# Kernel optimization log

Measured on AMD Instinct MI355X. Metric: run time of the kernel, lower is better.

Reference implementation:

```python
import jax, jax.numpy as jnp
import numpy as np

B, V, T = 8, 25, 128
C, NH, DK = 256, 8, 32      # hidden_size = NH*DK; dv == dk (required by residual shapes)
DFF, IT = 1024, 4           # FFN hidden (d_in), num_layers
EPS_LN, EPS_BN, SLOPE = 1e-6, 1e-5, 0.01
SCALE = np.float32(1.0 / np.sqrt(DK))


def setup_inputs():
    ks = iter(jax.random.split(jax.random.key(0), 40))
    def w(shape, s=0.05):
        return jax.random.normal(next(ks), shape, jnp.float32) * s
    inp = {'data': jax.random.normal(next(ks), (B, C, V, T), jnp.float32)}
    inp['ln_g'] = jnp.ones((IT, C)); inp['ln_b'] = jnp.zeros((IT, C))
    for p in ('tj', 'tr'):
        for nm in ('q', 'k', 'v'):
            inp[p + '_w' + nm] = w((IT, C, C))
            inp[p + '_b' + nm] = jnp.zeros((IT, C))
        inp[p + '_bn_g'] = jnp.ones((IT, C)); inp[p + '_bn_b'] = jnp.zeros((IT, C))
        inp[p + '_w1'] = w((IT, DFF, C)); inp[p + '_b1'] = jnp.zeros((IT, DFF))
        inp[p + '_w2'] = w((IT, C, DFF)); inp[p + '_b2'] = jnp.zeros((IT, C))
        inp[p + '_fbn_g'] = jnp.ones((IT, C)); inp[p + '_fbn_b'] = jnp.zeros((IT, C))
    return inp


def _bn(x, g, b, axes):
    # train-mode BatchNorm: batch stats, biased variance; channel axis = 1
    m = x.mean(axes, keepdims=True)
    v = ((x - m) ** 2).mean(axes, keepdims=True)
    sh = [1] * x.ndim; sh[1] = -1
    return (x - m) * jax.lax.rsqrt(v + EPS_BN) * g.reshape(sh) + b.reshape(sh)


def _ffn(x, w1, b1, w2, b2, fg, fb):
    # PositionFeedForward on x: [N, C, L] -> [N, C, L]
    xt = jnp.swapaxes(x, 1, 2)                                   # [N, L, C]
    h = jax.nn.relu(jnp.einsum('nlc,fc->nlf', xt, w1) + b1)
    o = jnp.einsum('nlf,cf->nlc', h, w2) + b2 + xt               # residual
    return _bn(jnp.swapaxes(o, 1, 2), fg, fb, (0, 2))


def _tju(x, ax, wq, bq, wk, bk, wv, bv, bn_g, bn_b, w1, b1, w2, b2, fg, fb):
    # sliding-window (3) self-attn + 2 relay tokens; x: [N,C,T], ax: [N,C,2,T]
    N = x.shape[0]
    q = (jnp.einsum('oc,nct->not', wq, x) + bq[:, None]).reshape(N, NH, DK, T)
    k = (jnp.einsum('oc,nct->not', wk, x) + bk[:, None]).reshape(N, NH, DK, T)
    v = (jnp.einsum('oc,nct->not', wv, x) + bv[:, None]).reshape(N, NH, DK, T)
    kp = jnp.pad(k, ((0, 0), (0, 0), (0, 0), (1, 1)))
    vp = jnp.pad(v, ((0, 0), (0, 0), (0, 0), (1, 1)))
    kw = jnp.stack([kp[..., u:u + T] for u in range(3)], axis=3)  # [N,NH,DK,3,T]
    vw = jnp.stack([vp[..., u:u + T] for u in range(3)], axis=3)
    ak = (jnp.einsum('oc,ncat->noat', wk, ax) + bk[:, None, None]).reshape(N, NH, DK, 2, T)
    av = (jnp.einsum('oc,ncat->noat', wv, ax) + bv[:, None, None]).reshape(N, NH, DK, 2, T)
    kk = jnp.concatenate([kw, ak], axis=3)                        # [N,NH,DK,5,T]
    vv = jnp.concatenate([vw, av], axis=3)
    a = jax.nn.softmax(jnp.einsum('nhdt,nhdwt->nhwt', q, kk) * SCALE, axis=2)
    att = jnp.einsum('nhwt,nhdwt->nhdt', a, vv).reshape(N, C, T)
    ret = _bn(x + att, bn_g, bn_b, (0, 2))
    return _ffn(ret, w1, b1, w2, b2, fg, fb)


def _tru(r, y, wq, bq, wk, bk, wv, bv, bn_g, bn_b, w1, b1, w2, b2, fg, fb):
    # relay cross-attention; r: [N,C], y: [N,C,L]
    N, _, L = y.shape
    q = (r @ wq.T + bq).reshape(N, NH, DK)
    k = (jnp.einsum('oc,ncl->nol', wk, y) + bk[:, None]).reshape(N, NH, DK, L)
    v = (jnp.einsum('oc,ncl->nol', wv, y) + bv[:, None]).reshape(N, NH, DK, L)
    a = jax.nn.softmax(jnp.einsum('nhd,nhdl->nhl', q, k) * SCALE, axis=-1)
    att = jnp.einsum('nhl,nhdl->nhd', a, v).reshape(N, C)
    ret = _bn((r + att)[:, :, None], bn_g, bn_b, (0, 2))          # BN over batch
    return _ffn(ret, w1, b1, w2, b2, fg, fb)[:, :, 0]


def _forward(data, ln_g, ln_b, tj, tr):
    N = B * V
    embs = jnp.transpose(data, (0, 2, 1, 3)).reshape(N, C, T)
    nodes, relay = embs, embs.mean(2)                             # relay: [N,C]
    for i in range(IT):
        ax = jnp.concatenate([embs[:, :, None, :],
                              jnp.broadcast_to(relay[:, :, None, None], (N, C, 1, T))], axis=2)
        m = nodes.mean(1, keepdims=True)
        vv = nodes.var(1, keepdims=True)
        xln = (nodes - m) * jax.lax.rsqrt(vv + EPS_LN) * ln_g[i][None, :, None] + ln_b[i][None, :, None]
        nodes = jax.nn.leaky_relu(_tju(xln, ax, *[p[i] for p in tj]), SLOPE)
        y = jnp.concatenate([relay[:, :, None], nodes], axis=2)   # [N,C,T+1]
        relay = jax.nn.leaky_relu(_tru(relay, y, *[p[i] for p in tr]), SLOPE)
    return nodes.reshape(B, V, C, T)


def reference(data, ln_g, ln_b,
              tj_wq, tj_bq, tj_wk, tj_bk, tj_wv, tj_bv, tj_bn_g, tj_bn_b,
              tj_w1, tj_b1, tj_w2, tj_b2, tj_fbn_g, tj_fbn_b,
              tr_wq, tr_bq, tr_wk, tr_bk, tr_wv, tr_bv, tr_bn_g, tr_bn_b,
              tr_w1, tr_b1, tr_w2, tr_b2, tr_fbn_g, tr_fbn_b):
    tj = (tj_wq, tj_bq, tj_wk, tj_bk, tj_wv, tj_bv, tj_bn_g, tj_bn_b,
          tj_w1, tj_b1, tj_w2, tj_b2, tj_fbn_g, tj_fbn_b)
    tr = (tr_wq, tr_bq, tr_wk, tr_bk, tr_wv, tr_bv, tr_bn_g, tr_bn_b,
          tr_w1, tr_b1, tr_w2, tr_b2, tr_fbn_g, tr_fbn_b)
    return _forward(data, ln_g, ln_b, tj, tr)
```

## Files before the change

### kernel.cpp

```cpp
#include <hip/hip_runtime.h>
#include <cstddef>

#define BB   8
#define VV   25
#define TT   128
#define CC   256
#define NHH  8
#define DKK  32
#define DFFF 1024
#define ITER 4
#define NN   (BB*VV)
#define NT   (NN*TT)
#define LL1  (TT+1)
#define EPS_LN 1e-6f
#define EPS_BN 1e-5f
#define SLOPE  0.01f
#define SCALE_F 0.17677669529663687f

typedef unsigned short ushort_t;
typedef __attribute__((ext_vector_type(8))) short short8;
typedef __attribute__((ext_vector_type(4))) short short4_t;
typedef __attribute__((ext_vector_type(4))) float floatx4;

union U8 { short8 v; ushort_t u[8]; };

__device__ __forceinline__ float bf2f(ushort_t u) {
    union { unsigned int i; float f; } x; x.i = ((unsigned int)u) << 16; return x.f;
}
__device__ __forceinline__ ushort_t f2bf(float f) {
    union { float f; unsigned int i; } x; x.f = f;
    unsigned int r = x.i + 0x7FFFu + ((x.i >> 16) & 1u);
    return (ushort_t)(r >> 16);
}
__device__ __forceinline__ float2 bn_fin(float s, float ss) {
    float m = s * (1.0f/NT);
    float var = ss * (1.0f/NT) - m*m; if (var < 0.f) var = 0.f;
    return make_float2(m, rsqrtf(var + EPS_BN));
}

__device__ __forceinline__ void gl_lds16(const ushort_t* g, ushort_t* l) {
    __builtin_amdgcn_global_load_lds(
        (const __attribute__((address_space(1))) unsigned int*)g,
        (__attribute__((address_space(3))) unsigned int*)l,
        16, 0, 0);
}

__device__ __forceinline__ void ld32(const ushort_t* p, float* q) {
    #pragma unroll
    for (int c8 = 0; c8 < 4; c8++) {
        U8 u; u.v = *(const short8*)(p + c8*8);
        #pragma unroll
        for (int j = 0; j < 8; j++) q[c8*8+j] = bf2f(u.u[j]);
    }
}
__device__ __forceinline__ float dot32(const ushort_t* p, const float* q) {
    float s = 0.f;
    #pragma unroll
    for (int c8 = 0; c8 < 4; c8++) {
        U8 u; u.v = *(const short8*)(p + c8*8);
        #pragma unroll
        for (int j = 0; j < 8; j++) s += q[c8*8+j]*bf2f(u.u[j]);
    }
    return s;
}
__device__ __forceinline__ void acc32(const ushort_t* p, float e, float* av) {
    #pragma unroll
    for (int c8 = 0; c8 < 4; c8++) {
        U8 u; u.v = *(const short8*)(p + c8*8);
        #pragma unroll
        for (int j = 0; j < 8; j++) av[c8*8+j] += e*bf2f(u.u[j]);
    }
}

__global__ __launch_bounds__(256) void k_zero(float* __restrict__ p, int n)
{
    int i = blockIdx.x*256 + threadIdx.x;
    if (i < n) p[i] = 0.f;
}
__global__ __launch_bounds__(256) void k_cast2(const float* __restrict__ src,
    ushort_t* __restrict__ dst, int per, int dstride, int total)
{
    int i = blockIdx.x*256 + threadIdx.x;
    if (i < total) dst[(size_t)(i/per)*dstride + (i%per)] = f2bf(src[i]);
}
__global__ __launch_bounds__(256) void k_copy2(const float* __restrict__ src,
    float* __restrict__ dst, int per, int dstride, int total)
{
    int i = blockIdx.x*256 + threadIdx.x;
    if (i < total) dst[(size_t)(i/per)*dstride + (i%per)] = src[i];
}

__global__ __launch_bounds__(128) void k_embed(const float* __restrict__ data,
    float* __restrict__ nodesf, ushort_t* __restrict__ embs_bf, float* __restrict__ relay)
{
    __shared__ float tile[32][TT+1];
    int cc0 = blockIdx.x*32, n = blockIdx.y;
    int b = n / VV, v = n % VV, t = threadIdx.x;
    for (int cl = 0; cl < 32; cl++)
        tile[cl][t] = data[(((size_t)b*CC + cc0 + cl)*VV + v)*TT + t];
    __syncthreads();
    if (t < 32) {
        float s = 0.f;
        for (int tt = 0; tt < TT; tt++) s += tile[t][tt];
        relay[n*CC + cc0 + t] = s * (1.0f/TT);
    }
    #pragma unroll 8
    for (int it = 0; it < 32; it++) {
        int t_l = it*4 + (t >> 5), c_l = t & 31;
        float val = tile[c_l][t_l];
        size_t o = (size_t)(n*TT + t_l)*CC + cc0 + c_l;
        nodesf[o] = val;
        embs_bf[o] = f2bf(val);
    }
}

__global__ __launch_bounds__(256) void k_layernorm(float* __restrict__ x,
    ushort_t* __restrict__ outb, const float* __restrict__ g, const float* __restrict__ b)
{
    int wave = threadIdx.x >> 6, lane = threadIdx.x & 63;
    size_t base = (size_t)(blockIdx.x*4 + wave)*CC + lane*4;
    float4 v = *(float4*)&x[base];
    float s  = v.x + v.y + v.z + v.w;
    float ss = v.x*v.x + v.y*v.y + v.z*v.z + v.w*v.w;
    #pragma unroll
    for (int o = 32; o; o >>= 1) { s += __shfl_xor(s, o); ss += __shfl_xor(ss, o); }
    float m = s * (1.0f/CC);
    float var = ss * (1.0f/CC) - m*m; if (var < 0.f) var = 0.f;
    float rs = rsqrtf(var + EPS_LN);
    float4 gg = *(const float4*)&g[lane*4];
    float4 bb = *(const float4*)&b[lane*4];
    v.x = (v.x - m)*rs*gg.x + bb.x;
    v.y = (v.y - m)*rs*gg.y + bb.y;
    v.z = (v.z - m)*rs*gg.z + bb.z;
    v.w = (v.w - m)*rs*gg.w + bb.w;
    *(float4*)&x[base] = v;
    ushort_t o4[4] = {f2bf(v.x), f2bf(v.y), f2bf(v.z), f2bf(v.w)};
    *(short4_t*)&outb[base] = *(short4_t*)o4;
}

#define FL_RELU  1
#define FL_BF16  2
#define FL_RESBN 4

#define STAGE(SA, SB, T_) do {                                              \
    gl_lds16(aSrc[0] + (T_)*32, &SA[dstOff[0]]);                            \
    gl_lds16(bSrc[0] + (T_)*32, &SB[dstOff[0]]);                            \
    gl_lds16(aSrc[1] + (T_)*32, &SA[dstOff[1]]);                            \
    gl_lds16(bSrc[1] + (T_)*32, &SB[dstOff[1]]);                            \
    } while (0)

#define COMPUTE(SA, SB) do {                                                \
    short8 af_[4], bf_[4];                                                  \
    _Pragma("unroll")                                                       \
    for (int mi_ = 0; mi_ < 4; mi_++)                                       \
        af_[mi_] = *(const short8*)&SA[aOff[mi_]];                          \
    _Pragma("unroll")                                                       \
    for (int ni_ = 0; ni_ < 4; ni_++)                                       \
        bf_[ni_] = *(const short8*)&SB[bOff[ni_]];                          \
    _Pragma("unroll")                                                       \
    for (int mi_ = 0; mi_ < 4; mi_++)                                       \
        _Pragma("unroll")                                                   \
        for (int ni_ = 0; ni_ < 4; ni_++)                                   \
            acc[mi_][ni_] = __builtin_amdgcn_mfma_f32_16x16x32_bf16(        \
                bf_[ni_], af_[mi_], acc[mi_][ni_], 0, 0, 0);                \
    } while (0)

#define PHASE(CA, CB, PA, PB, T_) do {                                      \
    if ((T_) + 2 < NK) STAGE(PA, PB, (T_) + 2);                             \
    COMPUTE(CA, CB);                                                        \
    if ((T_) + 1 < NK) {                                                    \
        __builtin_amdgcn_sched_barrier(0);                                  \
        if ((T_) + 2 < NK)                                                  \
            asm volatile("s_waitcnt vmcnt(4) lgkmcnt(0)" ::: "memory");     \
        else                                                                \
            asm volatile("s_waitcnt vmcnt(0) lgkmcnt(0)" ::: "memory");     \
        __builtin_amdgcn_s_barrier();                                       \
        __builtin_amdgcn_sched_barrier(0);                                  \
    }                                                                       \
    } while (0)

template<int K>
__global__ __launch_bounds__(256) void k_gemm_mfma(
    const ushort_t* __restrict__ A, const ushort_t* __restrict__ B,
    const float* __restrict__ bias,
    const float* rx, const float* __restrict__ rawms,
    const float* __restrict__ bng, const float* __restrict__ bnb,
    float* outf, ushort_t* __restrict__ outb,
    int ostride, int ntiles_n, int flags)
{
    __shared__ ushort_t sA0[128*32];
    __shared__ ushort_t sB0[128*32];
    __shared__ ushort_t sA1[128*32];
    __shared__ ushort_t sB1[128*32];
    __shared__ ushort_t sA2[128*32];
    __shared__ ushort_t sB2[128*32];
    const int pid = blockIdx.x;
    const int xcd = pid & 7, idx = pid >> 3;
    const int n0 = (idx % ntiles_n) * 128;
    const int m0 = (xcd*25 + idx/ntiles_n) * 128;
    const int tid = threadIdx.x;
    const int lane = tid & 63, wave = tid >> 6;
    const int wm = (wave & 1) * 64, wn = (wave >> 1) * 64;
    const int fr = lane >> 4, fc = lane & 15;

    const ushort_t* aSrc[2];
    const ushort_t* bSrc[2];
    int dstOff[2];
    #pragma unroll
    for (int j = 0; j < 2; j++) {
        int s = wave*128 + j*64 + lane;
        int row = s >> 2;
        int kcs = ((s & 3) - (row >> 1)) & 3;
        aSrc[j] = A + (size_t)(m0 + row)*K + kcs*8;
        bSrc[j] = B + (size_t)(n0 + row)*K + kcs*8;
        dstOff[j] = (wave*128 + j*64)*8;
    }
    int aOff[4], bOff[4];
    #pragma unroll
    for (int mi = 0; mi < 4; mi++) {
        int row = wm + mi*16 + fc;
        aOff[mi] = row*32 + (((fr + (row >> 1)) & 3) * 8);
    }
    #pragma unroll
    for (int ni = 0; ni < 4; ni++) {
        int row = wn + ni*16 + fc;
        bOff[ni] = row*32 + (((fr + (row >> 1)) & 3) * 8);
    }

    floatx4 acc[4][4];
    #pragma unroll
    for (int i = 0; i < 4; i++)
        #pragma unroll
        for (int j = 0; j < 4; j++) acc[i][j] = (floatx4){0.f,0.f,0.f,0.f};

    constexpr int NK = K >> 5;
    STAGE(sA0, sB0, 0);
    if (NK > 1) STAGE(sA1, sB1, 1);
    __builtin_amdgcn_sched_barrier(0);
    if (NK > 1) asm volatile("s_waitcnt vmcnt(4)" ::: "memory");
    else        asm volatile("s_waitcnt vmcnt(0)" ::: "memory");
    __builtin_amdgcn_s_barrier();
    __builtin_amdgcn_sched_barrier(0);

    #pragma unroll
    for (int tb = 0; tb < NK; tb += 3) {
        PHASE(sA0, sB0, sA2, sB2, tb);
        if (tb + 1 < NK) PHASE(sA1, sB1, sA0, sB0, tb + 1);
        if (tb + 2 < NK) PHASE(sA2, sB2, sA1, sB1, tb + 2);
    }

    #pragma unroll
    for (int ni = 0; ni < 4; ni++) {
        int nb = n0 + wn + ni*16 + fr*4;
        float4 bias4 = *(const float4*)&bias[nb];
        float bm[4] = {0,0,0,0}, bs[4] = {0,0,0,0}, bb2[4] = {0,0,0,0};
        if (flags & FL_RESBN) {
            float4 s1 = *(const float4*)&rawms[nb];
            float4 s2 = *(const float4*)&rawms[CC + nb];
            float4 g4 = *(const float4*)&bng[nb];
            float4 b4 = *(const float4*)&bnb[nb];
            float2 f0 = bn_fin(s1.x, s2.x); float2 f1 = bn_fin(s1.y, s2.y);
            float2 f2 = bn_fin(s1.z, s2.z); float2 f3 = bn_fin(s1.w, s2.w);
            bm[0]=f0.x; bm[1]=f1.x; bm[2]=f2.x; bm[3]=f3.x;
            bs[0]=f0.y*g4.x; bs[1]=f1.y*g4.y; bs[2]=f2.y*g4.z; bs[3]=f3.y*g4.w;
            bb2[0]=b4.x; bb2[1]=b4.y; bb2[2]=b4.z; bb2[3]=b4.w;
        }
        float bia[4] = {bias4.x, bias4.y, bias4.z, bias4.w};
        #pragma unroll
        for (int mi = 0; mi < 4; mi++) {
            int m = m0 + wm + mi*16 + fc;
            size_t idx2 = (size_t)m*ostride + nb;
            float vals[4];
            #pragma unroll
            for (int r = 0; r < 4; r++) vals[r] = acc[mi][ni][r] + bia[r];
            if (flags & FL_RESBN) {
                float4 rx4 = *(const float4*)&rx[idx2];
                float rxa[4] = {rx4.x, rx4.y, rx4.z, rx4.w};
                #pragma unroll
                for (int r = 0; r < 4; r++)
                    vals[r] += (rxa[r] - bm[r])*bs[r] + bb2[r];
            }
            if (flags & FL_RELU)
                #pragma unroll
                for (int r = 0; r < 4; r++) vals[r] = fmaxf(vals[r], 0.f);
            if (flags & FL_BF16) {
                ushort_t o4[4] = {f2bf(vals[0]), f2bf(vals[1]),
                                  f2bf(vals[2]), f2bf(vals[3])};
                *(short4_t*)&outb[idx2] = *(short4_t*)o4;
            } else {
                float4 ov = make_float4(vals[0], vals[1], vals[2], vals[3]);
                *(float4*)&outf[idx2] = ov;
            }
        }
    }
}

__global__ __launch_bounds__(256) void k_sgemm(
    const float* __restrict__ W, const float* __restrict__ X,
    const float* __restrict__ bias, const float* __restrict__ res,
    float* __restrict__ out, int K, int OUT, int do_relu)
{
    __shared__ float sW[16][260];
    __shared__ float sX[16][260];
    int o0 = blockIdx.x*16, n0 = blockIdx.y*16;
    int tx = threadIdx.x, ty = threadIdx.y;
    int tid = ty*16 + tx;
    float acc0 = 0.f, acc1 = 0.f;
    for (int kc = 0; kc < K; kc += 256) {
        #pragma unroll
        for (int j = 0; j < 4; j++) {
            int lin = tid + j*256;
            int row = lin >> 6, c4 = (lin & 63)*4;
            *(float4*)&sW[row][c4] = *(const float4*)&W[(size_t)(o0+row)*K + kc + c4];
            float4 xv = make_float4(0.f,0.f,0.f,0.f);
            if (n0 + row < NN) xv = *(const float4*)&X[(size_t)(n0+row)*K + kc + c4];
            *(float4*)&sX[row][c4] = xv;
        }
        __syncthreads();
        #pragma unroll 8
        for (int k4 = 0; k4 < 64; k4 += 2) {
            float4 w0 = *(const float4*)&sW[tx][k4*4];
            float4 x0 = *(const float4*)&sX[ty][k4*4];
            float4 w1 = *(const float4*)&sW[tx][k4*4+4];
            float4 x1 = *(const float4*)&sX[ty][k4*4+4];
            acc0 += w0.x*x0.x + w0.y*x0.y + w0.z*x0.z + w0.w*x0.w;
            acc1 += w1.x*x1.x + w1.y*x1.y + w1.z*x1.z + w1.w*x1.w;
        }
        __syncthreads();
    }
    float accv = acc0 + acc1;
    int o = o0 + tx, n = n0 + ty;
    if (n < NN) {
        float val = accv + bias[o];
        if (res) val += res[(size_t)n*OUT + o];
        if (do_relu) val = fmaxf(val, 0.f);
        out[(size_t)n*OUT + o] = val;
    }
}

__global__ __launch_bounds__(128) void k_attn_tj(
    const ushort_t* __restrict__ qkv, const ushort_t* __restrict__ ekv,
    const float* __restrict__ rel, const float* __restrict__ xln,
    float* __restrict__ out)
{
    int t = threadIdx.x, h = blockIdx.x, n = blockIdx.y;
    int nt = n*TT + t;
    const ushort_t* qp = qkv + (size_t)nt*768 + h*32;
    const ushort_t* kp = qp + 256;
    const ushort_t* vp = qp + 512;
    const ushort_t* ep = ekv + (size_t)nt*512 + h*32;
    const float*    rp = rel + n*1280 + h*32;

    float qv[32];
    ld32(qp, qv);
    float s0 = 0.f, s1, s2 = 0.f, s3, s4 = 0.f;
    s1 = dot32(kp, qv);
    s3 = dot32(ep, qv);
    #pragma unroll
    for (int j = 0; j < 8; j++) {
        float4 rv4 = *(const float4*)&rp[j*4];
        s4 += qv[j*4]*rv4.x + qv[j*4+1]*rv4.y + qv[j*4+2]*rv4.z + qv[j*4+3]*rv4.w;
    }
    if (t > 0)    s0 = dot32(kp - 768, qv);
    if (t < TT-1) s2 = dot32(kp + 768, qv);

    s0 *= SCALE_F; s1 *= SCALE_F; s2 *= SCALE_F; s3 *= SCALE_F; s4 *= SCALE_F;
    float mx = fmaxf(fmaxf(fmaxf(s0, s1), fmaxf(s2, s3)), s4);
    float e0 = expf(s0-mx), e1 = expf(s1-mx), e2 = expf(s2-mx), e3 = expf(s3-mx), e4 = expf(s4-mx);
    float inv = 1.f/(e0+e1+e2+e3+e4);
    e0 *= inv; e1 *= inv; e2 *= inv; e3 *= inv; e4 *= inv;

    float av[32];
    #pragma unroll
    for (int d = 0; d < 32; d++) av[d] = 0.f;
    acc32(vp, e1, av);
    acc32(ep + 256, e3, av);
    if (t > 0)    acc32(vp - 768, e0, av);
    if (t < TT-1) acc32(vp + 768, e2, av);
    #pragma unroll
    for (int j = 0; j < 8; j++) {
        float4 rv4 = *(const float4*)&rp[256 + j*4];
        av[j*4] += e4*rv4.x; av[j*4+1] += e4*rv4.y; av[j*4+2] += e4*rv4.z; av[j*4+3] += e4*rv4.w;
    }
    const float* xp = xln + (size_t)nt*CC + h*32;
    float* op = out + (size_t)nt*CC + h*32;
    #pragma unroll
    for (int j = 0; j < 8; j++) {
        float4 xv = *(const float4*)&xp[j*4];
        float4 ov;
        ov.x = xv.x + av[j*4]; ov.y = xv.y + av[j*4+1];
        ov.z = xv.z + av[j*4+2]; ov.w = xv.w + av[j*4+3];
        *(float4*)&op[j*4] = ov;
    }
}

__global__ __launch_bounds__(256) void k_bnstats_tm(const float* __restrict__ x,
    float* __restrict__ accum)
{
    __shared__ float lds[8][256];
    int w = threadIdx.x >> 6, lane = threadIdx.x & 63;
    size_t base = (size_t)blockIdx.x*TT*CC;
    float s[4] = {0,0,0,0}, ss[4] = {0,0,0,0};
    for (int tok = w; tok < TT; tok += 4) {
        float4 v = *(const float4*)&x[base + (size_t)tok*CC + lane*4];
        s[0] += v.x; s[1] += v.y; s[2] += v.z; s[3] += v.w;
        ss[0] += v.x*v.x; ss[1] += v.y*v.y; ss[2] += v.z*v.z; ss[3] += v.w*v.w;
    }
    #pragma unroll
    for (int j = 0; j < 4; j++) { lds[w][lane*4+j] = s[j]; lds[4+w][lane*4+j] = ss[j]; }
    __syncthreads();
    int c = threadIdx.x;
    float ps  = lds[0][c]+lds[1][c]+lds[2][c]+lds[3][c];
    float pss = lds[4][c]+lds[5][c]+lds[6][c]+lds[7][c];
    atomicAdd(&accum[c], ps);
    atomicAdd(&accum[CC + c], pss);
}

__global__ __launch_bounds__(256) void k_bn_apply_raw(const float* __restrict__ x,
    const float* __restrict__ acc, const float* __restrict__ g, const float* __restrict__ b,
    ushort_t* __restrict__ outb)
{
    size_t base = ((size_t)blockIdx.x*256 + threadIdx.x)*4;
    int c0 = (int)(base & (CC-1));
    float4 v  = *(const float4*)&x[base];
    float4 a1 = *(const float4*)&acc[c0];
    float4 a2 = *(const float4*)&acc[CC + c0];
    float4 g4 = *(const float4*)&g[c0];
    float4 b4 = *(const float4*)&b[c0];
    float vals[4] = {v.x,v.y,v.z,v.w};
    float s1v[4] = {a1.x,a1.y,a1.z,a1.w};
    float s2v[4] = {a2.x,a2.y,a2.z,a2.w};
    float gg[4] = {g4.x,g4.y,g4.z,g4.w};
    float bb[4] = {b4.x,b4.y,b4.z,b4.w};
    ushort_t o4[4];
    #pragma unroll
    for (int j = 0; j < 4; j++) {
        float2 f = bn_fin(s1v[j], s2v[j]);
        o4[j] = f2bf((vals[j] - f.x)*f.y*gg[j] + bb[j]);
    }
    *(short4_t*)&outb[base] = *(short4_t*)o4;
}

__global__ __launch_bounds__(256) void k_bn_ln(const float* __restrict__ x,
    const float* __restrict__ acc, const float* __restrict__ fg, const float* __restrict__ fb,
    const float* __restrict__ lg, const float* __restrict__ lb,
    float* __restrict__ xlnf, ushort_t* __restrict__ xlnb, ushort_t* __restrict__ nodesb)
{
    int wave = threadIdx.x >> 6, lane = threadIdx.x & 63;
    int c0 = lane*4;
    size_t base = (size_t)(blockIdx.x*4 + wave)*CC + c0;
    float4 v  = *(const float4*)&x[base];
    float4 a1 = *(const float4*)&acc[c0];
    float4 a2 = *(const float4*)&acc[CC + c0];
    float4 g4 = *(const float4*)&fg[c0];
    float4 b4 = *(const float4*)&fb[c0];
    float vals[4] = {v.x,v.y,v.z,v.w};
    float s1v[4] = {a1.x,a1.y,a1.z,a1.w};
    float s2v[4] = {a2.x,a2.y,a2.z,a2.w};
    float gg[4] = {g4.x,g4.y,g4.z,g4.w};
    float bb[4] = {b4.x,b4.y,b4.z,b4.w};
    ushort_t nb4[4];
    #pragma unroll
    for (int j = 0; j < 4; j++) {
        float2 f = bn_fin(s1v[j], s2v[j]);
        float vv = (vals[j] - f.x)*f.y*gg[j] + bb[j];
        vv = vv > 0.f ? vv : SLOPE*vv;
        vals[j] = vv;
        nb4[j] = f2bf(vv);
    }
    *(short4_t*)&nodesb[base] = *(short4_t*)nb4;
    float s  = vals[0]+vals[1]+vals[2]+vals[3];
    float ss = vals[0]*vals[0]+vals[1]*vals[1]+vals[2]*vals[2]+vals[3]*vals[3];
    #pragma unroll
    for (int o = 32; o; o >>= 1) { s += __shfl_xor(s, o); ss += __shfl_xor(ss, o); }
    float m = s * (1.0f/CC);
    float var = ss * (1.0f/CC) - m*m; if (var < 0.f) var = 0.f;
    float rs = rsqrtf(var + EPS_LN);
    float4 lg4 = *(const float4*)&lg[c0];
    float4 lb4 = *(const float4*)&lb[c0];
    float lgv[4] = {lg4.x,lg4.y,lg4.z,lg4.w};
    float lbv[4] = {lb4.x,lb4.y,lb4.z,lb4.w};
    float4 xo;
    ushort_t xb4[4];
    float t0 = (vals[0]-m)*rs*lgv[0] + lbv[0];
    float t1 = (vals[1]-m)*rs*lgv[1] + lbv[1];
    float t2 = (vals[2]-m)*rs*lgv[2] + lbv[2];
    float t3 = (vals[3]-m)*rs*lgv[3] + lbv[3];
    xo.x = t0; xo.y = t1; xo.z = t2; xo.w = t3;
    xb4[0]=f2bf(t0); xb4[1]=f2bf(t1); xb4[2]=f2bf(t2); xb4[3]=f2bf(t3);
    *(float4*)&xlnf[base] = xo;
    *(short4_t*)&xlnb[base] = *(short4_t*)xb4;
}

__global__ __launch_bounds__(256) void k_bn_out_t(const float* __restrict__ x,
    const float* __restrict__ acc, const float* __restrict__ g, const float* __restrict__ b,
    float* __restrict__ out)
{
    __shared__ float tile[64][65];
    int nt0 = blockIdx.x*64, c0 = blockIdx.y*64;
    int w = threadIdx.x >> 6, lane = threadIdx.x & 63;
    int n = nt0 >> 7, t0 = nt0 & 127;
    int c = c0 + lane;
    float2 f = bn_fin(acc[c], acc[CC + c]);
    float gg = f.y*g[c], mm = f.x, bb = b[c];
    #pragma unroll
    for (int it = 0; it < 16; it++) {
        int tok = it*4 + w;
        float v = x[(size_t)(nt0 + tok)*CC + c];
        v = (v - mm)*gg + bb;
        v = v > 0.f ? v : SLOPE*v;
        tile[tok][lane] = v;
    }
    __syncthreads();
    #pragma unroll
    for (int it = 0; it < 16; it++) {
        int c_l = it*4 + w;
        out[(size_t)(n*CC + c0 + c_l)*TT + t0 + lane] = tile[lane][c_l];
    }
}

__global__ __launch_bounds__(64) void k_bn_relay(const float* __restrict__ x,
    float* __restrict__ out, const float* __restrict__ g, const float* __restrict__ b, int leaky)
{
    int c = blockIdx.x, tid = threadIdx.x;
    float s = 0.f, ss = 0.f;
    for (int n = tid; n < NN; n += 64) { float v = x[(size_t)n*CC + c]; s += v; ss += v*v; }
    for (int off = 32; off; off >>= 1) { s += __shfl_down(s, off); ss += __shfl_down(ss, off); }
    float S = __shfl(s, 0), SS = __shfl(ss, 0);
    float m = S / NN;
    float var = SS / NN - m*m; if (var < 0.f) var = 0.f;
    float rs = rsqrtf(var + EPS_BN);
    float gg = g[c]*rs, bb = b[c];
    for (int n = tid; n < NN; n += 64) {
        float v = (x[(size_t)n*CC + c] - m)*gg + bb;
        if (leaky) v = v > 0.f ? v : SLOPE*v;
        out[(size_t)n*CC + c] = v;
    }
}

__global__ __launch_bounds__(64) void k_attn_tr(
    const float* __restrict__ rel, const float* __restrict__ ykv,
    const float* __restrict__ relay, float* __restrict__ out)
{
    int h = blockIdx.x, n = blockIdx.y, tid = threadIdx.x;
    __shared__ float sc[LL1];
    __shared__ float red[64][33];
    float q0[32];
    const float* qp = rel + (size_t)n*1280 + 1024 + h*32;
    #pragma unroll
    for (int j = 0; j < 8; j++) {
        float4 v = *(const float4*)&qp[j*4];
        q0[j*4] = v.x; q0[j*4+1] = v.y; q0[j*4+2] = v.z; q0[j*4+3] = v.w;
    }
    for (int l = tid; l < LL1; l += 64) {
        const float* kp = (l == 0) ? (rel + (size_t)n*1280 + 512 + h*32)
                                   : (ykv + (size_t)(n*TT + l-1)*512 + h*32);
        float s = 0.f;
        #pragma unroll
        for (int j = 0; j < 8; j++) {
            float4 v = *(const float4*)&kp[j*4];
            s += q0[j*4]*v.x + q0[j*4+1]*v.y + q0[j*4+2]*v.z + q0[j*4+3]*v.w;
        }
        sc[l] = s * SCALE_F;
    }
    __syncthreads();
    float mx = -1e30f;
    for (int l = tid; l < LL1; l += 64) mx = fmaxf(mx, sc[l]);
    for (int off = 32; off; off >>= 1) mx = fmaxf(mx, __shfl_xor(mx, off));
    float sum = 0.f;
    for (int l = tid; l < LL1; l += 64) { float e = expf(sc[l]-mx); sc[l] = e; sum += e; }
    for (int off = 32; off; off >>= 1) sum += __shfl_xor(sum, off);
    __syncthreads();
    float av[32];
    #pragma unroll
    for (int d = 0; d < 32; d++) av[d] = 0.f;
    for (int l = tid; l < LL1; l += 64) {
        float e = sc[l];
        const float* vp = (l == 0) ? (rel + (size_t)n*1280 + 768 + h*32)
                                   : (ykv + (size_t)(n*TT + l-1)*512 + 256 + h*32);
        #pragma unroll
        for (int j = 0; j < 8; j++) {
            float4 v = *(const float4*)&vp[j*4];
            av[j*4] += e*v.x; av[j*4+1] += e*v.y; av[j*4+2] += e*v.z; av[j*4+3] += e*v.w;
        }
    }
    #pragma unroll
    for (int d = 0; d < 32; d++) red[tid][d] = av[d];
    __syncthreads();
    if (tid < 32) {
        float a = 0.f;
        for (int k = 0; k < 64; k++) a += red[k][tid];
        a /= sum;
        int idx = n*CC + h*32 + tid;
        out[idx] = relay[idx] + a;
    }
}

extern "C" void kernel_launch(void* const* d_in, const int* in_sizes, int n_in,
                              void* d_out, int out_size, void* d_ws, size_t ws_size,
                              hipStream_t stream)
{
    const float* data    = (const float*)d_in[0];
    const float* ln_g    = (const float*)d_in[1];
    const float* ln_b    = (const float*)d_in[2];
    const float* tj_wq   = (const float*)d_in[3];
    const float* tj_bq   = (const float*)d_in[4];
    const float* tj_wk   = (const float*)d_in[5];
    const float* tj_bk   = (const float*)d_in[6];
    const float* tj_wv   = (const float*)d_in[7];
    const float* tj_bv   = (const float*)d_in[8];
    const float* tj_bn_g = (const float*)d_in[9];
    const float* tj_bn_b = (const float*)d_in[10];
    const float* tj_w1   = (const float*)d_in[11];
    const float* tj_b1   = (const float*)d_in[12];
    const float* tj_w2   = (const float*)d_in[13];
    const float* tj_b2   = (const float*)d_in[14];
    const float* tj_fbn_g= (const float*)d_in[15];
    const float* tj_fbn_b= (const float*)d_in[16];
    const float* tr_wq   = (const float*)d_in[17];
    const float* tr_bq   = (const float*)d_in[18];
    const float* tr_wk   = (const float*)d_in[19];
    const float* tr_bk   = (const float*)d_in[20];
    const float* tr_wv   = (const float*)d_in[21];
    const float* tr_bv   = (const float*)d_in[22];
    const float* tr_bn_g = (const float*)d_in[23];
    const float* tr_bn_b = (const float*)d_in[24];
    const float* tr_w1   = (const float*)d_in[25];
    const float* tr_b1   = (const float*)d_in[26];
    const float* tr_w2   = (const float*)d_in[27];
    const float* tr_b2   = (const float*)d_in[28];
    const float* tr_fbn_g= (const float*)d_in[29];
    const float* tr_fbn_b= (const float*)d_in[30];

    const size_t SZ = (size_t)NT*CC;
    const size_t SZ_NC = (size_t)NN*CC;

    float* ws = (float*)d_ws;
    size_t off = 0;
    auto alloc = [&](size_t nf) { float* p = ws + off; off += nf; return p; };
    float*    nodesf  = alloc(SZ);
    float*    sbuf    = alloc(SZ);
    float*    P1      = alloc(SZ*5/2);
    ushort_t* xs_bf   = (ushort_t*)alloc(SZ/2);
    ushort_t* embs_bf = (ushort_t*)alloc(SZ/2);
    ushort_t* nb_bf   = (ushort_t*)alloc(SZ/2);
    float* accs   = alloc(8*512);
    float* relayA = alloc(SZ_NC);
    float* relayB = alloc(SZ_NC);
    float* rel    = alloc((size_t)NN*1280);
    float* ret0   = alloc(SZ_NC);
    float* rret   = alloc(SZ_NC);
    float* ro     = alloc(SZ_NC);
    float* rh     = alloc((size_t)NN*DFFF);
    ushort_t* wqkv_bf  = (ushort_t*)alloc((size_t)ITER*768*CC/2);
    ushort_t* wkvtr_bf = (ushort_t*)alloc((size_t)ITER*512*CC/2);
    ushort_t* w1_bf    = (ushort_t*)alloc((size_t)ITER*DFFF*CC/2);
    ushort_t* w2_bf    = (ushort_t*)alloc((size_t)ITER*DFFF*CC/2);
    float* wrel  = alloc((size_t)ITER*1280*CC);
    float* brel  = alloc((size_t)ITER*1280);
    float* bqkv  = alloc((size_t)ITER*768);
    float* bkvtr = alloc((size_t)ITER*512);
    (void)ws_size; (void)in_sizes; (void)n_in; (void)out_size;

    ushort_t* qkv_tm = (ushort_t*)P1;
    ushort_t* ekv_tm = qkv_tm + 3*SZ;
    ushort_t* h_us   = (ushort_t*)P1;
    float*    ykv_f  = P1;

    const int TCC = ITER*CC*CC, TFF = ITER*DFFF*CC;
    k_zero<<<16, 256, 0, stream>>>(accs, 8*512);
    k_cast2<<<(TCC+255)/256, 256, 0, stream>>>(tj_wq, wqkv_bf,          65536, 196608, TCC);
    k_cast2<<<(TCC+255)/256, 256, 0, stream>>>(tj_wk, wqkv_bf +  65536, 65536, 196608, TCC);
    k_cast2<<<(TCC+255)/256, 256, 0, stream>>>(tj_wv, wqkv_bf + 131072, 65536, 196608, TCC);
    k_cast2<<<(TCC+255)/256, 256, 0, stream>>>(tr_wk, wkvtr_bf,         65536, 131072, TCC);
    k_cast2<<<(TCC+255)/256, 256, 0, stream>>>(tr_wv, wkvtr_bf + 65536, 65536, 131072, TCC);
    k_cast2<<<(TFF+255)/256, 256, 0, stream>>>(tj_w1, w1_bf, TFF, TFF, TFF);
    k_cast2<<<(TFF+255)/256, 256, 0, stream>>>(tj_w2, w2_bf, TFF, TFF, TFF);
    k_copy2<<<(ITER*256+255)/256, 256, 0, stream>>>(tj_bq, bqkv,       256, 768, ITER*256);
    k_copy2<<<(ITER*256+255)/256, 256, 0, stream>>>(tj_bk, bqkv + 256, 256, 768, ITER*256);
    k_copy2<<<(ITER*256+255)/256, 256, 0, stream>>>(tj_bv, bqkv + 512, 256, 768, ITER*256);
    k_copy2<<<(ITER*256+255)/256, 256, 0, stream>>>(tr_bk, bkvtr,      256, 512, ITER*256);
    k_copy2<<<(ITER*256+255)/256, 256, 0, stream>>>(tr_bv, bkvtr+256,  256, 512, ITER*256);
    k_copy2<<<(TCC+255)/256, 256, 0, stream>>>(tj_wk, wrel,          65536, 327680, TCC);
    k_copy2<<<(TCC+255)/256, 256, 0, stream>>>(tj_wv, wrel +  65536, 65536, 327680, TCC);
    k_copy2<<<(TCC+255)/256, 256, 0, stream>>>(tr_wk, wrel + 131072, 65536, 327680, TCC);
    k_copy2<<<(TCC+255)/256, 256, 0, stream>>>(tr_wv, wrel + 196608, 65536, 327680, TCC);
    k_copy2<<<(TCC+255)/256, 256, 0, stream>>>(tr_wq, wrel + 262144, 65536, 327680, TCC);
    k_copy2<<<(ITER*256+255)/256, 256, 0, stream>>>(tj_bk, brel,        256, 1280, ITER*256);
    k_copy2<<<(ITER*256+255)/256, 256, 0, stream>>>(tj_bv, brel +  256, 256, 1280, ITER*256);
    k_copy2<<<(ITER*256+255)/256, 256, 0, stream>>>(tr_bk, brel +  512, 256, 1280, ITER*256);
    k_copy2<<<(ITER*256+255)/256, 256, 0, stream>>>(tr_bv, brel +  768, 256, 1280, ITER*256);
    k_copy2<<<(ITER*256+255)/256, 256, 0, stream>>>(tr_bq, brel + 1024, 256, 1280, ITER*256);

    k_embed<<<dim3(8, NN), 128, 0, stream>>>(data, nodesf, embs_bf, relayA);
    k_layernorm<<<NT/4, 256, 0, stream>>>(nodesf, xs_bf, ln_g, ln_b);

    float* relay = relayA;
    float* relay_next = relayB;
    dim3 sb16(16, 16);

    for (int i = 0; i < ITER; i++) {
        const size_t woff = (size_t)i*DFFF*CC;
        float* accA = accs + i*1024;
        float* accB = accs + i*1024 + 512;

        k_sgemm<<<dim3((i == ITER-1) ? 32 : 80, 13), sb16, 0, stream>>>(
            wrel + (size_t)i*1280*CC, relay, brel + i*1280, nullptr, rel, CC, 1280, 0);

        k_gemm_mfma<256><<<200*6, 256, 0, stream>>>(
            xs_bf, wqkv_bf + (size_t)i*768*CC, bqkv + i*768, nullptr, nullptr, nullptr, nullptr,
            nullptr, qkv_tm, 768, 6, FL_BF16);
        k_gemm_mfma<256><<<200*4, 256, 0, stream>>>(
            embs_bf, wqkv_bf + (size_t)i*768*CC + 65536, bqkv + i*768 + 256,
            nullptr, nullptr, nullptr, nullptr,
            nullptr, ekv_tm, 512, 4, FL_BF16);

        k_attn_tj<<<dim3(NHH, NN), 128, 0, stream>>>(qkv_tm, ekv_tm, rel, nodesf, sbuf);

        k_bnstats_tm<<<NN, 256, 0, stream>>>(sbuf, accA);
        k_bn_apply_raw<<<SZ/1024, 256, 0, stream>>>(
            sbuf, accA, tj_bn_g + i*CC, tj_bn_b + i*CC, xs_bf);

        k_gemm_mfma<256><<<200*8, 256, 0, stream>>>(
            xs_bf, w1_bf + woff, tj_b1 + i*DFFF, nullptr, nullptr, nullptr, nullptr,
            nullptr, h_us, DFFF, 8, FL_RELU | FL_BF16);
        k_gemm_mfma<1024><<<200*2, 256, 0, stream>>>(
            h_us, w2_bf + woff, tj_b2 + i*CC, sbuf, accA, tj_bn_g + i*CC, tj_bn_b + i*CC,
            sbuf, nullptr, CC, 2, FL_RESBN);

        k_bnstats_tm<<<NN, 256, 0, stream>>>(sbuf, accB);
        if (i == ITER-1) {
            k_bn_out_t<<<dim3(NT/64, CC/64), 256, 0, stream>>>(
                sbuf, accB, tj_fbn_g + i*CC, tj_fbn_b + i*CC, (float*)d_out);
            break;
        }
        k_bn_ln<<<NT/4, 256, 0, stream>>>(
            sbuf, accB, tj_fbn_g + i*CC, tj_fbn_b + i*CC,
            ln_g + (i+1)*CC, ln_b + (i+1)*CC, nodesf, xs_bf, nb_bf);

        k_gemm_mfma<256><<<200*4, 256, 0, stream>>>(
            nb_bf, wkvtr_bf + (size_t)i*512*CC, bkvtr + i*512,
            nullptr, nullptr, nullptr, nullptr,
            ykv_f, nullptr, 512, 4, 0);

        k_attn_tr<<<dim3(NHH, NN), 64, 0, stream>>>(rel, ykv_f, relay, ret0);
        k_bn_relay<<<CC, 64, 0, stream>>>(ret0, rret, tr_bn_g + i*CC, tr_bn_b + i*CC, 0);

        k_sgemm<<<dim3(DFFF/16, (NN+15)/16), sb16, 0, stream>>>(
            tr_w1 + woff, rret, tr_b1 + i*DFFF, nullptr, rh, CC, DFFF, 1);
        k_sgemm<<<dim3(16, (NN+15)/16), sb16, 0, stream>>>(
            tr_w2 + woff, rh, tr_b2 + i*CC, rret, ro, DFFF, CC, 0);
        k_bn_relay<<<CC, 64, 0, stream>>>(ro, relay_next, tr_fbn_g + i*CC, tr_fbn_b + i*CC, 1);

        float* tmp = relay; relay = relay_next; relay_next = tmp;
    }
}
```

Baseline: 1.230 ms.

## Fuse BN statistics into attention and GEMM epilogues, merge QKV/EKV GEMMs

Removes the separate k_bnstats_tm passes. BatchNorm sum and sum-of-squares are now accumulated inside the tj attention kernel, through an LDS transpose and atomics, and inside the FFN2 GEMM epilogue, through shuffle reductions and atomics. The two projection GEMMs (QKV on xs and KV on embeddings) are merged into one launch that picks operands per tile. This avoids two full reads of the activation buffer and two kernel launches per layer. The cost is extra epilogue work, more atomics, and the loss of __restrict__ on some GEMM pointers.

```diff
diff --git a/kernel.cpp b/kernel.cpp
--- a/kernel.cpp
+++ b/kernel.cpp
@@ -179,14 +179,15 @@
     }                                                                       \
     } while (0)
 
-template<int K>
+template<int K, int STATS>
 __global__ __launch_bounds__(256) void k_gemm_mfma(
-    const ushort_t* __restrict__ A, const ushort_t* __restrict__ B,
-    const float* __restrict__ bias,
+    const ushort_t* A, const ushort_t* B, const float* bias,
     const float* rx, const float* __restrict__ rawms,
     const float* __restrict__ bng, const float* __restrict__ bnb,
-    float* outf, ushort_t* __restrict__ outb,
-    int ostride, int ntiles_n, int flags)
+    float* outf, ushort_t* outb, int ostride, int ntiles_n, int flags,
+    const ushort_t* A2, const ushort_t* B2, const float* bias2,
+    ushort_t* outb2, int ostride2, int ntiles_n2,
+    float* stats_acc)
 {
     __shared__ ushort_t sA0[128*32];
     __shared__ ushort_t sB0[128*32];
@@ -196,8 +197,18 @@
     __shared__ ushort_t sB2[128*32];
     const int pid = blockIdx.x;
     const int xcd = pid & 7, idx = pid >> 3;
-    const int n0 = (idx % ntiles_n) * 128;
-    const int m0 = (xcd*25 + idx/ntiles_n) * 128;
+    const int ntile_tot = ntiles_n + ntiles_n2;
+    const int nt_i = idx % ntile_tot;
+    const int m0 = (xcd*25 + idx/ntile_tot) * 128;
+    const ushort_t* Ap;  const ushort_t* Bp;  const float* biasp;
+    ushort_t* outbp;  int ostridep, n0;
+    if (nt_i < ntiles_n) {
+        Ap = A;  Bp = B;  biasp = bias;  outbp = outb;
+        ostridep = ostride;  n0 = nt_i*128;
+    } else {
+        Ap = A2; Bp = B2; biasp = bias2; outbp = outb2;
+        ostridep = ostride2; n0 = (nt_i - ntiles_n)*128;
+    }
     const int tid = threadIdx.x;
     const int lane = tid & 63, wave = tid >> 6;
     const int wm = (wave & 1) * 64, wn = (wave >> 1) * 64;
@@ -211,8 +222,8 @@
         int s = wave*128 + j*64 + lane;
         int row = s >> 2;
         int kcs = ((s & 3) - (row >> 1)) & 3;
-        aSrc[j] = A + (size_t)(m0 + row)*K + kcs*8;
-        bSrc[j] = B + (size_t)(n0 + row)*K + kcs*8;
+        aSrc[j] = Ap + (size_t)(m0 + row)*K + kcs*8;
+        bSrc[j] = Bp + (size_t)(n0 + row)*K + kcs*8;
         dstOff[j] = (wave*128 + j*64)*8;
     }
     int aOff[4], bOff[4];
@@ -249,10 +260,17 @@
         if (tb + 2 < NK) PHASE(sA2, sB2, sA1, sB1, tb + 2);
     }
 
+    float st[4][4], sst[4][4];
+    if constexpr (STATS) {
+        #pragma unroll
+        for (int a = 0; a < 4; a++)
+            #pragma unroll
+            for (int b2_ = 0; b2_ < 4; b2_++) { st[a][b2_] = 0.f; sst[a][b2_] = 0.f; }
+    }
     #pragma unroll
     for (int ni = 0; ni < 4; ni++) {
         int nb = n0 + wn + ni*16 + fr*4;
-        float4 bias4 = *(const float4*)&bias[nb];
+        float4 bias4 = *(const float4*)&biasp[nb];
         float bm[4] = {0,0,0,0}, bs[4] = {0,0,0,0}, bb2[4] = {0,0,0,0};
         if (flags & FL_RESBN) {
             float4 s1 = *(const float4*)&rawms[nb];
@@ -269,7 +287,7 @@
         #pragma unroll
         for (int mi = 0; mi < 4; mi++) {
             int m = m0 + wm + mi*16 + fc;
-            size_t idx2 = (size_t)m*ostride + nb;
+            size_t idx2 = (size_t)m*ostridep + nb;
             float vals[4];
             #pragma unroll
             for (int r = 0; r < 4; r++) vals[r] = acc[mi][ni][r] + bia[r];
@@ -283,14 +301,45 @@
             if (flags & FL_RELU)
                 #pragma unroll
                 for (int r = 0; r < 4; r++) vals[r] = fmaxf(vals[r], 0.f);
+            if constexpr (STATS) {
+                #pragma unroll
+                for (int r = 0; r < 4; r++) {
+                    st[ni][r] += vals[r];
+                    sst[ni][r] += vals[r]*vals[r];
+                }
+            }
             if (flags & FL_BF16) {
                 ushort_t o4[4] = {f2bf(vals[0]), f2bf(vals[1]),
                                   f2bf(vals[2]), f2bf(vals[3])};
-                *(short4_t*)&outb[idx2] = *(short4_t*)o4;
+                *(short4_t*)&outbp[idx2] = *(short4_t*)o4;
             } else {
                 float4 ov = make_float4(vals[0], vals[1], vals[2], vals[3]);
                 *(float4*)&outf[idx2] = ov;
             }
+        }
+    }
+    if constexpr (STATS) {
+        #pragma unroll
+        for (int ni = 0; ni < 4; ni++)
+            #pragma unroll
+            for (int r = 0; r < 4; r++) {
+                float s_ = st[ni][r], ss_ = sst[ni][r];
+                #pragma unroll
+                for (int msk = 1; msk < 16; msk <<= 1) {
+                    s_  += __shfl_xor(s_,  msk);
+                    ss_ += __shfl_xor(ss_, msk);
+                }
+                st[ni][r] = s_; sst[ni][r] = ss_;
+            }
+        if (fc == 0) {
+            #pragma unroll
+            for (int ni = 0; ni < 4; ni++)
+                #pragma unroll
+                for (int r = 0; r < 4; r++) {
+                    int ch = n0 + wn + ni*16 + fr*4 + r;
+                    atomicAdd(&stats_acc[ch],      st[ni][r]);
+                    atomicAdd(&stats_acc[CC + ch], sst[ni][r]);
+                }
         }
     }
 }
@@ -341,8 +390,9 @@
 __global__ __launch_bounds__(128) void k_attn_tj(
     const ushort_t* __restrict__ qkv, const ushort_t* __restrict__ ekv,
     const float* __restrict__ rel, const float* __restrict__ xln,
-    float* __restrict__ out)
-{
+    float* __restrict__ out, float* __restrict__ accum)
+{
+    __shared__ float svals[128][33];
     int t = threadIdx.x, h = blockIdx.x, n = blockIdx.y;
     int nt = n*TT + t;
     const ushort_t* qp = qkv + (size_t)nt*768 + h*32;
@@ -391,29 +441,20 @@
         ov.x = xv.x + av[j*4]; ov.y = xv.y + av[j*4+1];
         ov.z = xv.z + av[j*4+2]; ov.w = xv.w + av[j*4+3];
         *(float4*)&op[j*4] = ov;
-    }
-}
-
-__global__ __launch_bounds__(256) void k_bnstats_tm(const float* __restrict__ x,
-    float* __restrict__ accum)
-{
-    __shared__ float lds[8][256];
-    int w = threadIdx.x >> 6, lane = threadIdx.x & 63;
-    size_t base = (size_t)blockIdx.x*TT*CC;
-    float s[4] = {0,0,0,0}, ss[4] = {0,0,0,0};
-    for (int tok = w; tok < TT; tok += 4) {
-        float4 v = *(const float4*)&x[base + (size_t)tok*CC + lane*4];
-        s[0] += v.x; s[1] += v.y; s[2] += v.z; s[3] += v.w;
-        ss[0] += v.x*v.x; ss[1] += v.y*v.y; ss[2] += v.z*v.z; ss[3] += v.w*v.w;
-    }
-    #pragma unroll
-    for (int j = 0; j < 4; j++) { lds[w][lane*4+j] = s[j]; lds[4+w][lane*4+j] = ss[j]; }
+        svals[t][j*4+0] = ov.x; svals[t][j*4+1] = ov.y;
+        svals[t][j*4+2] = ov.z; svals[t][j*4+3] = ov.w;
+    }
     __syncthreads();
-    int c = threadIdx.x;
-    float ps  = lds[0][c]+lds[1][c]+lds[2][c]+lds[3][c];
-    float pss = lds[4][c]+lds[5][c]+lds[6][c]+lds[7][c];
-    atomicAdd(&accum[c], ps);
-    atomicAdd(&accum[CC + c], pss);
+    if (t < 64) {
+        int ch = t & 31, seg = t >> 5;
+        float s = 0.f, ss = 0.f;
+        for (int r = 0; r < 64; r++) {
+            float v = svals[seg*64 + r][ch];
+            s += v; ss += v*v;
+        }
+        atomicAdd(&accum[h*32 + ch], s);
+        atomicAdd(&accum[CC + h*32 + ch], ss);
+    }
 }
 
 __global__ __launch_bounds__(256) void k_bn_apply_raw(const float* __restrict__ x,
@@ -707,28 +748,27 @@
         k_sgemm<<<dim3((i == ITER-1) ? 32 : 80, 13), sb16, 0, stream>>>(
             wrel + (size_t)i*1280*CC, relay, brel + i*1280, nullptr, rel, CC, 1280, 0);
 
-        k_gemm_mfma<256><<<200*6, 256, 0, stream>>>(
-            xs_bf, wqkv_bf + (size_t)i*768*CC, bqkv + i*768, nullptr, nullptr, nullptr, nullptr,
-            nullptr, qkv_tm, 768, 6, FL_BF16);
-        k_gemm_mfma<256><<<200*4, 256, 0, stream>>>(
+        k_gemm_mfma<256,0><<<200*10, 256, 0, stream>>>(
+            xs_bf, wqkv_bf + (size_t)i*768*CC, bqkv + i*768,
+            nullptr, nullptr, nullptr, nullptr,
+            nullptr, qkv_tm, 768, 6, FL_BF16,
             embs_bf, wqkv_bf + (size_t)i*768*CC + 65536, bqkv + i*768 + 256,
-            nullptr, nullptr, nullptr, nullptr,
-            nullptr, ekv_tm, 512, 4, FL_BF16);
-
-        k_attn_tj<<<dim3(NHH, NN), 128, 0, stream>>>(qkv_tm, ekv_tm, rel, nodesf, sbuf);
-
-        k_bnstats_tm<<<NN, 256, 0, stream>>>(sbuf, accA);
+            ekv_tm, 512, 4, nullptr);
+
+        k_attn_tj<<<dim3(NHH, NN), 128, 0, stream>>>(qkv_tm, ekv_tm, rel, nodesf, sbuf, accA);
+
         k_bn_apply_raw<<<SZ/1024, 256, 0, stream>>>(
             sbuf, accA, tj_bn_g + i*CC, tj_bn_b + i*CC, xs_bf);
 
-        k_gemm_mfma<256><<<200*8, 256, 0, stream>>>(
+        k_gemm_mfma<256,0><<<200*8, 256, 0, stream>>>(
             xs_bf, w1_bf + woff, tj_b1 + i*DFFF, nullptr, nullptr, nullptr, nullptr,
-            nullptr, h_us, DFFF, 8, FL_RELU | FL_BF16);
-        k_gemm_mfma<1024><<<200*2, 256, 0, stream>>>(
+            nullptr, h_us, DFFF, 8, FL_RELU | FL_BF16,
+            nullptr, nullptr, nullptr, nullptr, 0, 0, nullptr);
+        k_gemm_mfma<1024,1><<<200*2, 256, 0, stream>>>(
             h_us, w2_bf + woff, tj_b2 + i*CC, sbuf, accA, tj_bn_g + i*CC, tj_bn_b + i*CC,
-            sbuf, nullptr, CC, 2, FL_RESBN);
-
-        k_bnstats_tm<<<NN, 256, 0, stream>>>(sbuf, accB);
+            sbuf, nullptr, CC, 2, FL_RESBN,
+            nullptr, nullptr, nullptr, nullptr, 0, 0, accB);
+
         if (i == ITER-1) {
             k_bn_out_t<<<dim3(NT/64, CC/64), 256, 0, stream>>>(
                 sbuf, accB, tj_fbn_g + i*CC, tj_fbn_b + i*CC, (float*)d_out);
@@ -738,10 +778,11 @@
             sbuf, accB, tj_fbn_g + i*CC, tj_fbn_b + i*CC,
             ln_g + (i+1)*CC, ln_b + (i+1)*CC, nodesf, xs_bf, nb_bf);
 
-        k_gemm_mfma<256><<<200*4, 256, 0, stream>>>(
+        k_gemm_mfma<256,0><<<200*4, 256, 0, stream>>>(
             nb_bf, wkvtr_bf + (size_t)i*512*CC, bkvtr + i*512,
             nullptr, nullptr, nullptr, nullptr,
-            ykv_f, nullptr, 512, 4, 0);
+            ykv_f, nullptr, 512, 4, 0,
+            nullptr, nullptr, nullptr, nullptr, 0, 0, nullptr);
 
         k_attn_tr<<<dim3(NHH, NN), 64, 0, stream>>>(rel, ykv_f, relay, ret0);
         k_bn_relay<<<CC, 64, 0, stream>>>(ret0, rret, tr_bn_g + i*CC, tr_bn_b + i*CC, 0);
```

After: 1.275 ms. 3.7% more time.
